# Optimization experiments

Hardware: AMD Instinct MI355X
Metric: run time of the kernel (lower is better)

## Reference

```python
import jax, jax.numpy as jnp
import numpy as np

NHID = 128; NUM_CLASSES = 128; NUM_CONVS = 3; EDGE_RATIO = 0.8
B_GRAPHS = 256; N_PER_G = 256; E_PER_G = 512
N_TOTAL = B_GRAPHS * N_PER_G; E_TOTAL = B_GRAPHS * E_PER_G
ATOM_DIMS = [119, 4, 12, 12, 10, 6, 6, 2, 2]
BOND_DIMS = [5, 6, 2]


def setup_inputs():
    key = jax.random.key(0)
    ks = jax.random.split(key, 32)
    a_off = np.concatenate([[0], np.cumsum(ATOM_DIMS)[:-1]])
    x_idx = jnp.stack([jax.random.randint(ks[i], (N_TOTAL,), 0, dm) + int(o)
                       for i, (dm, o) in enumerate(zip(ATOM_DIMS, a_off))], axis=1)
    b_off = np.concatenate([[0], np.cumsum(BOND_DIMS)[:-1]])
    edge_attr_idx = jnp.stack([jax.random.randint(ks[9 + i], (E_TOTAL,), 0, dm) + int(o)
                               for i, (dm, o) in enumerate(zip(BOND_DIMS, b_off))], axis=1)
    # block-structured edges: each graph's edges are contiguous, endpoints local
    src = jax.random.randint(ks[12], (B_GRAPHS, E_PER_G), 0, N_PER_G)
    dst = jax.random.randint(ks[13], (B_GRAPHS, E_PER_G), 0, N_PER_G)
    off = jnp.arange(B_GRAPHS)[:, None] * N_PER_G
    edge_index = jnp.stack([(src + off).reshape(-1), (dst + off).reshape(-1)])
    batch = jnp.repeat(jnp.arange(B_GRAPHS), N_PER_G)
    s = 0.05
    d = NHID
    def rn(k, shape):
        return jax.random.normal(k, shape, dtype=jnp.float32) * s
    return {
        "x_idx": x_idx, "edge_attr_idx": edge_attr_idx,
        "edge_index": edge_index, "batch": batch,
        "atom_table": rn(ks[14], (sum(ATOM_DIMS), d)),
        "bond_table": rn(ks[15], (sum(BOND_DIMS), d)),
        "W_gcn": rn(ks[16], (NUM_CONVS, d, d)), "b_gcn": rn(ks[17], (NUM_CONVS, d)),
        "root_emb": rn(ks[18], (NUM_CONVS, d)),
        "W_hyp": rn(ks[19], (NUM_CONVS - 1, d, d)), "b_hyp": rn(ks[20], (NUM_CONVS - 1, d)),
        "W_sc": rn(ks[21], (NUM_CONVS - 1, d, 1)), "b_sc": rn(ks[22], (NUM_CONVS - 1, 1)),
        "Wc1": rn(ks[23], (3 * d, d)), "bc1": rn(ks[24], (d,)),
        "Wc2": rn(ks[25], (d, d // 2)), "bc2": rn(ks[26], (d // 2,)),
        "Wc3": rn(ks[27], (d // 2, NUM_CLASSES)), "bc3": rn(ks[28], (NUM_CLASSES,)),
    }


def reference(x_idx, edge_attr_idx, edge_index, batch, atom_table, bond_table,
              W_gcn, b_gcn, root_emb, W_hyp, b_hyp, W_sc, b_sc,
              Wc1, bc1, Wc2, bc2, Wc3, bc3):
    seg = jax.ops.segment_sum
    x = atom_table[x_idx].sum(axis=1)          # [N, d] AtomEncoder: sum of per-feature embeddings
    e = bond_table[edge_attr_idx].sum(axis=1)  # [E, d] BondEncoder
    edge_weight = None
    xs = 0.0
    for l in range(NUM_CONVS):
        E = edge_index.shape[1]
        # ---- DHT: dual hypergraph (edges -> nodes, nodes -> hyperedges), with loops & degree-1 mask
        flat = edge_index.T.reshape(-1)  # [2E] node ids in (src,dst,src,dst,...) order
        node_idx = jnp.concatenate([jnp.repeat(jnp.arange(E), 2), jnp.arange(E)])       # [3E]
        hyper_idx = jnp.concatenate([flat, N_TOTAL + jnp.arange(E)])                    # [3E]
        bc = seg(jnp.ones(2 * E, jnp.float32), flat, num_segments=N_TOTAL)
        mask = jnp.concatenate([bc[flat] != 1.0, jnp.ones((E,), dtype=bool)])
        w = mask.astype(x.dtype)
        NH = N_TOTAL + E
        # ---- GCNConv_OGB
        row, col = edge_index[0], edge_index[1]
        h = x @ W_gcn[l] + b_gcn[l]
        deg = seg(jnp.ones(E, x.dtype), row, num_segments=N_TOTAL) + 1.0
        dis = deg ** -0.5
        msg = (dis[row] * dis[col])[:, None] * jax.nn.relu(h[row] + e)
        if edge_weight is not None:
            msg = msg * edge_weight[:, None]
        x = jax.nn.relu(seg(msg, col, num_segments=N_TOTAL)
                        + jax.nn.relu(h + root_emb[l]) / deg[:, None])
        if l < NUM_CONVS - 1:
            # ---- HypergraphConv on edge features (nodes of dual = original edges)
            Dn = seg(w, node_idx, num_segments=E)
            Bh = seg(w, hyper_idx, num_segments=NH)
            Dinv = jnp.where(Dn > 0, 1.0 / Dn, 0.0)
            Binv = jnp.where(Bh > 0, 1.0 / Bh, 0.0)
            def hconv(feat, W, b):
                z = feat @ W
                m = seg(z[node_idx] * w[:, None], hyper_idx, num_segments=NH) * Binv[:, None]
                return seg(m[hyper_idx] * w[:, None], node_idx, num_segments=E) * Dinv[:, None] + b
            e = jax.nn.relu(hconv(e, W_hyp[l], b_hyp[l]))
            score = jnp.tanh(hconv(e, W_sc[l], b_sc[l]).squeeze(-1))  # [E]
            # ---- topk edge pooling (uniform per-graph blocks -> static k)
            Eg = E // B_GRAPHS
            k = int(np.ceil(EDGE_RATIO * Eg))
            _, loc = jax.lax.top_k(score.reshape(B_GRAPHS, Eg), k)
            perm = (loc + jnp.arange(B_GRAPHS)[:, None] * Eg).reshape(-1)
            edge_index = edge_index[:, perm]
            e = e[perm]
            edge_weight = jnp.clip(score[perm], 0.0, 1.0)
        # ---- readout: gmp | gap | gsp  (uniform graphs -> reshape)
        xr = x.reshape(B_GRAPHS, N_PER_G, NHID)
        xs = xs + jnp.concatenate([xr.max(axis=1), xr.mean(axis=1), xr.sum(axis=1)], axis=1)
    # ---- classifier (eval mode: dropout is identity)
    h1 = jax.nn.relu(xs @ Wc1 + bc1)
    h2 = jax.nn.relu(h1 @ Wc2 + bc2)
    return h2 @ Wc3 + bc3
```

## Files before the change

kernel.cpp:

```cpp
#include <hip/hip_runtime.h>
#include <hip/hip_bf16.h>
#include <math.h>

constexpr int NTOT = 65536;
constexpr int D    = 128;
constexpr int BG   = 256;
constexpr int E0 = 131072, E1 = 104960, E2 = 83968;
constexpr int EG0 = 512;
constexpr int KP0 = 410, KP1 = 328;

typedef __bf16 bf16x8 __attribute__((ext_vector_type(8)));
typedef __bf16 bf16x4 __attribute__((ext_vector_type(4)));
typedef __bf16 bf16x2 __attribute__((ext_vector_type(2)));
typedef float  f32x4  __attribute__((ext_vector_type(4)));

__device__ __forceinline__ float2 tof2(bf16x2 v) {
  return make_float2((float)v[0], (float)v[1]);
}
__device__ __forceinline__ bf16x2 tob2(float ax, float ay) {
  bf16x2 r; r[0] = (__bf16)ax; r[1] = (__bf16)ay; return r;
}

__global__ __launch_bounds__(256) void k_embed_x(const int* __restrict__ xi,
                                                 const float* __restrict__ tab,
                                                 __bf16* __restrict__ x) {
  int t = blockIdx.x * 256 + threadIdx.x;
  int v = t >> 5, q = (t & 31) << 2;
  float4 s = {0.f, 0.f, 0.f, 0.f};
#pragma unroll
  for (int j = 0; j < 9; ++j) {
    int r = xi[v * 9 + j];
    float4 a = *(const float4*)&tab[r * D + q];
    s.x += a.x; s.y += a.y; s.z += a.z; s.w += a.w;
  }
  bf16x4 o; o[0] = (__bf16)s.x; o[1] = (__bf16)s.y; o[2] = (__bf16)s.z; o[3] = (__bf16)s.w;
  *(bf16x4*)&x[(size_t)v * D + q] = o;
}

__global__ __launch_bounds__(256) void k_embed_e(const int* __restrict__ bi,
                                                 const float* __restrict__ tab,
                                                 __bf16* __restrict__ e) {
  int t = blockIdx.x * 256 + threadIdx.x;
  int i = t >> 5, q = (t & 31) << 2;
  float4 s = {0.f, 0.f, 0.f, 0.f};
#pragma unroll
  for (int j = 0; j < 3; ++j) {
    int r = bi[i * 3 + j];
    float4 a = *(const float4*)&tab[r * D + q];
    s.x += a.x; s.y += a.y; s.z += a.z; s.w += a.w;
  }
  bf16x4 o; o[0] = (__bf16)s.x; o[1] = (__bf16)s.y; o[2] = (__bf16)s.z; o[3] = (__bf16)s.w;
  *(bf16x4*)&e[(size_t)i * D + q] = o;
}

__global__ __launch_bounds__(256) void k_gemm_bf16(const __bf16* __restrict__ A,
                                                   const float* __restrict__ W,
                                                   const float* __restrict__ bias,
                                                   __bf16* __restrict__ C) {
  __shared__ bf16x8 Wl[4][8][64];
  const int t = threadIdx.x, w = t >> 6, lane = t & 63;
  const int m0 = blockIdx.x * 128;

  bf16x8* Wf = (bf16x8*)Wl;
  for (int q = t; q < 2048; q += 256) {
    int ks = q >> 9, nt = (q >> 6) & 7, l = q & 63;
    int kk = ks * 32 + ((l >> 4) << 3);
    int nn = nt * 16 + (l & 15);
    const float* wp = W + (size_t)kk * 128 + nn;
    bf16x8 v;
#pragma unroll
    for (int b = 0; b < 8; ++b) v[b] = (__bf16)wp[(size_t)b * 128];
    Wf[q] = v;
  }

  const int r0 = m0 + w * 32 + (lane & 15);
  const __bf16* Ap0 = A + (size_t)r0 * 128 + ((lane >> 4) << 3);
  const __bf16* Ap1 = Ap0 + 16 * 128;
  bf16x8 a0[4], a1[4];
#pragma unroll
  for (int ks = 0; ks < 4; ++ks) {
    a0[ks] = *(const bf16x8*)(Ap0 + ks * 32);
    a1[ks] = *(const bf16x8*)(Ap1 + ks * 32);
  }
  __syncthreads();

  f32x4 acc0[8] = {}; f32x4 acc1[8] = {};
#pragma unroll
  for (int ks = 0; ks < 4; ++ks) {
#pragma unroll
    for (int nt = 0; nt < 8; ++nt) {
      bf16x8 b = Wl[ks][nt][lane];
      acc0[nt] = __builtin_amdgcn_mfma_f32_16x16x32_bf16(a0[ks], b, acc0[nt], 0, 0, 0);
      acc1[nt] = __builtin_amdgcn_mfma_f32_16x16x32_bf16(a1[ks], b, acc1[nt], 0, 0, 0);
    }
  }

  const int orow = m0 + w * 32 + ((lane >> 4) << 2);
  const int ocol = lane & 15;
#pragma unroll
  for (int nt = 0; nt < 8; ++nt) {
    float bb = bias ? bias[nt * 16 + ocol] : 0.f;
    __bf16* cp = C + (size_t)orow * 128 + nt * 16 + ocol;
#pragma unroll
    for (int r = 0; r < 4; ++r) {
      cp[(size_t)r * 128]        = (__bf16)(acc0[nt][r] + bb);
      cp[(size_t)(16 + r) * 128] = (__bf16)(acc1[nt][r] + bb);
    }
  }
}

template <int EG, bool HAS_EW>
__global__ __launch_bounds__(1024, 4) void k_gcn_fused(const int* __restrict__ ei, int E,
                                                       const __bf16* __restrict__ e,
                                                       const float* __restrict__ Wg,
                                                       const float* __restrict__ bg,
                                                       const float* __restrict__ ew,
                                                       const float* __restrict__ root,
                                                       __bf16* __restrict__ x,
                                                       float* __restrict__ xs) {
  constexpr int NW = 16;
  __shared__ bf16x8 Wl[4][8][64];
  __shared__ __bf16 hl[256 * 128];
  __shared__ int   pke[EG];
  __shared__ float coef[EG];
  __shared__ int   cnts[256];
  __shared__ int   cntd[256];
  __shared__ int   off[257];
  __shared__ int   cur[256];
  __shared__ int   wsum[4];
  __shared__ short adj[EG];
  __shared__ float redm[16 * 128], reds[16 * 128];
  const int g = blockIdx.x;
  const int t = threadIdx.x, w = t >> 6, lane = t & 63;
  const bf16x2* eg2 = (const bf16x2*)e + (size_t)g * EG * 64 + lane;
  bf16x2* xg2 = (bf16x2*)x + (size_t)g * 256 * 64 + lane;

  if (t < 256) { cnts[t] = 0; cntd[t] = 0; }
  __syncthreads();

  for (int j = t; j < EG; j += 1024) {
    int s = ei[g * EG + j] & 255, d = ei[E + g * EG + j] & 255;
    pke[j] = s | (d << 8);
    atomicAdd(&cnts[s], 1);
    atomicAdd(&cntd[d], 1);
  }
  {
    bf16x8* Wf = (bf16x8*)Wl;
    for (int q = t; q < 2048; q += 1024) {
      int ks = q >> 9, nt = (q >> 6) & 7, l = q & 63;
      int kk = ks * 32 + ((l >> 4) << 3);
      int nn = nt * 16 + (l & 15);
      const float* wp = Wg + (size_t)kk * 128 + nn;
      bf16x8 v;
#pragma unroll
      for (int b = 0; b < 8; ++b) v[b] = (__bf16)wp[(size_t)b * 128];
      Wf[q] = v;
    }
  }
  __syncthreads();

  {
    const int r0 = w * 16 + (lane & 15);
    const __bf16* Ap = x + ((size_t)(g * 256 + r0)) * 128 + ((lane >> 4) << 3);
    bf16x8 af[4];
#pragma unroll
    for (int ks = 0; ks < 4; ++ks) af[ks] = *(const bf16x8*)(Ap + ks * 32);
    f32x4 acc[8] = {};
#pragma unroll
    for (int ks = 0; ks < 4; ++ks) {
#pragma unroll
      for (int nt = 0; nt < 8; ++nt) {
        acc[nt] = __builtin_amdgcn_mfma_f32_16x16x32_bf16(af[ks], Wl[ks][nt][lane], acc[nt], 0, 0, 0);
      }
    }
    const int lrow = w * 16 + ((lane >> 4) << 2);
    const int ocol = lane & 15;
#pragma unroll
    for (int nt = 0; nt < 8; ++nt) {
      float bb = bg[nt * 16 + ocol];
#pragma unroll
      for (int r = 0; r < 4; ++r)
        hl[(lrow + r) * 128 + nt * 16 + ocol] = (__bf16)(acc[nt][r] + bb);
    }
  }

  for (int j = t; j < EG; j += 1024) {
    int p = pke[j];
    int s = p & 255, d = (p >> 8) & 255;
    float c = rsqrtf(((float)cnts[s] + 1.f) * ((float)cnts[d] + 1.f));
    if (HAS_EW) c *= ew[g * EG + j];
    coef[j] = c;
  }

  {
    int v = 0;
    if (t < 256) {
      v = cntd[t];
#pragma unroll
      for (int d2 = 1; d2 < 64; d2 <<= 1) {
        int u = __shfl_up(v, d2);
        if (lane >= d2) v += u;
      }
      if (lane == 63) wsum[w] = v;
    }
    __syncthreads();
    if (t < 256) {
      int add = 0;
      if (w > 0) add += wsum[0];
      if (w > 1) add += wsum[1];
      if (w > 2) add += wsum[2];
      off[t + 1] = v + add;
      if (t == 0) off[0] = 0;
      cur[t] = v + add - cntd[t];
    }
    __syncthreads();
  }

  for (int j = t; j < EG; j += 1024) {
    int d = (pke[j] >> 8) & 255;
    int pos = atomicAdd(&cur[d], 1);
    adj[pos] = (short)j;
  }
  __syncthreads();

  const float rvx = root[2 * lane], rvy = root[2 * lane + 1];
  float2 mx = {-1e30f, -1e30f}, sm = {0.f, 0.f};
  for (int n = w; n < 256; n += NW) {
    float2 val = {0.f, 0.f};
    int b0 = off[n], b1 = off[n + 1];
    int k = b0;
    for (; k + 1 < b1; k += 2) {
      int j0 = adj[k], j1 = adj[k + 1];
      int s0 = pke[j0] & 255, s1 = pke[j1] & 255;
      float2 e0 = tof2(eg2[(size_t)j0 * 64]), e1 = tof2(eg2[(size_t)j1 * 64]);
      float2 h0 = tof2(*(const bf16x2*)&hl[s0 * 128 + 2 * lane]);
      float2 h1 = tof2(*(const bf16x2*)&hl[s1 * 128 + 2 * lane]);
      float c0 = coef[j0], c1 = coef[j1];
      val.x += c0 * fmaxf(h0.x + e0.x, 0.f) + c1 * fmaxf(h1.x + e1.x, 0.f);
      val.y += c0 * fmaxf(h0.y + e0.y, 0.f) + c1 * fmaxf(h1.y + e1.y, 0.f);
    }
    if (k < b1) {
      int j0 = adj[k];
      int s0 = pke[j0] & 255;
      float2 e0 = tof2(eg2[(size_t)j0 * 64]);
      float2 h0 = tof2(*(const bf16x2*)&hl[s0 * 128 + 2 * lane]);
      float c0 = coef[j0];
      val.x += c0 * fmaxf(h0.x + e0.x, 0.f);
      val.y += c0 * fmaxf(h0.y + e0.y, 0.f);
    }
    float inv = 1.f / ((float)cnts[n] + 1.f);
    float2 hv = tof2(*(const bf16x2*)&hl[n * 128 + 2 * lane]);
    float xvx = fmaxf(val.x + fmaxf(hv.x + rvx, 0.f) * inv, 0.f);
    float xvy = fmaxf(val.y + fmaxf(hv.y + rvy, 0.f) * inv, 0.f);
    xg2[(size_t)n * 64] = tob2(xvx, xvy);
    mx.x = fmaxf(mx.x, xvx); mx.y = fmaxf(mx.y, xvy);
    sm.x += xvx;             sm.y += xvy;
  }
  redm[w * 128 + 2 * lane]     = mx.x;
  redm[w * 128 + 2 * lane + 1] = mx.y;
  reds[w * 128 + 2 * lane]     = sm.x;
  reds[w * 128 + 2 * lane + 1] = sm.y;
  __syncthreads();

  if (t < 128) {
    float M = redm[t], S2 = reds[t];
#pragma unroll
    for (int k = 1; k < 16; ++k) {
      M = fmaxf(M, redm[k * 128 + t]);
      S2 += reds[k * 128 + t];
    }
    xs[g * 384 + t]       += M;
    xs[g * 384 + 128 + t] += S2 * (1.f / 256.f);
    xs[g * 384 + 256 + t] += S2;
  }
}

template <int EG, int KEEP, int ENEW>
__global__ __launch_bounds__(1024, 4) void k_hyper_sort(const int* __restrict__ ei, int E,
                                                        const __bf16* __restrict__ z,
                                                        const float* __restrict__ bias,
                                                        const float* __restrict__ wsc,
                                                        const float* __restrict__ bsc,
                                                        __bf16* __restrict__ eout,
                                                        int* __restrict__ ei_new,
                                                        __bf16* __restrict__ e_new,
                                                        float* __restrict__ ew) {
  constexpr int NW = 16;
  __shared__ __bf16 S[256 * 128];
  __shared__ int   pke[EG];
  __shared__ float as_[EG], ad_[EG], az_[EG];
  __shared__ float zsh[EG];
  __shared__ float Ssh[256];
  __shared__ int   cnt[256];
  __shared__ int   off[257];
  __shared__ int   cur[256];
  __shared__ int   wsum[4];
  __shared__ short adj[2 * EG];
  __shared__ float ls[512];
  __shared__ int   li[512];
  __shared__ int   sidx[512];
  const int g = blockIdx.x;
  const int t = threadIdx.x, w = t >> 6, lane = t & 63;
  const bf16x2* zg2 = (const bf16x2*)z + (size_t)g * EG * 64 + lane;
  bf16x2* eo2 = (bf16x2*)eout + (size_t)g * EG * 64 + lane;
  bf16x2* S2 = (bf16x2*)S;

  if (t < 256) { cnt[t] = 0; Ssh[t] = 0.f; }
  __syncthreads();

  for (int j = t; j < EG; j += 1024) {
    int s = ei[g * EG + j] & 255, d = ei[E + g * EG + j] & 255;
    pke[j] = s | (d << 8);
    atomicAdd(&cnt[s], 1);
    atomicAdd(&cnt[d], 1);
  }
  __syncthreads();

  for (int j = t; j < EG; j += 1024) {
    int p = pke[j];
    int s = p & 255, d = (p >> 8) & 255;
    int cs = cnt[s], cd = cnt[d];
    float bis  = (cs != 1) ? 1.f / (float)cs : 0.f;
    float bid_ = (cd != 1) ? 1.f / (float)cd : 0.f;
    float dinv = 1.f / (1.f + (cs != 1 ? 1.f : 0.f) + (cd != 1 ? 1.f : 0.f));
    as_[j] = dinv * bis;
    ad_[j] = dinv * bid_;
    az_[j] = dinv;
  }

  {
    int v = 0;
    if (t < 256) {
      v = cnt[t];
#pragma unroll
      for (int d2 = 1; d2 < 64; d2 <<= 1) {
        int u = __shfl_up(v, d2);
        if (lane >= d2) v += u;
      }
      if (lane == 63) wsum[w] = v;
    }
    __syncthreads();
    if (t < 256) {
      int add = 0;
      if (w > 0) add += wsum[0];
      if (w > 1) add += wsum[1];
      if (w > 2) add += wsum[2];
      off[t + 1] = v + add;
      if (t == 0) off[0] = 0;
      cur[t] = v + add - cnt[t];
    }
    __syncthreads();
  }

  for (int j = t; j < EG; j += 1024) {
    int p = pke[j];
    int pos0 = atomicAdd(&cur[p & 255], 1);
    adj[pos0] = (short)j;
    int pos1 = atomicAdd(&cur[(p >> 8) & 255], 1);
    adj[pos1] = (short)j;
  }
  __syncthreads();

  for (int n = w; n < 256; n += NW) {
    float2 val = {0.f, 0.f};
    int b0 = off[n], b1 = off[n + 1];
    int k = b0;
    for (; k + 1 < b1; k += 2) {
      float2 a = tof2(zg2[(size_t)adj[k] * 64]);
      float2 b = tof2(zg2[(size_t)adj[k + 1] * 64]);
      val.x += a.x + b.x;
      val.y += a.y + b.y;
    }
    if (k < b1) {
      float2 a = tof2(zg2[(size_t)adj[k] * 64]);
      val.x += a.x; val.y += a.y;
    }
    S2[n * 64 + lane] = tob2(val.x, val.y);
  }
  __syncthreads();

  const float bbx = bias[2 * lane], bby = bias[2 * lane + 1];
  const float wvx = wsc[2 * lane],  wvy = wsc[2 * lane + 1];
  for (int j = w; j < EG; j += NW) {
    int p = pke[j];
    int s = p & 255, d = (p >> 8) & 255;
    float a_s = as_[j], a_d = ad_[j], a_z = az_[j];
    float2 Sv = tof2(S2[s * 64 + lane]);
    float2 Dv = tof2(S2[d * 64 + lane]);
    float2 zv = tof2(zg2[(size_t)j * 64]);
    float ox = fmaxf(a_s * Sv.x + a_d * Dv.x + a_z * zv.x + bbx, 0.f);
    float oy = fmaxf(a_s * Sv.y + a_d * Dv.y + a_z * zv.y + bby, 0.f);
    eo2[(size_t)j * 64] = tob2(ox, oy);
    float part = ox * wvx + oy * wvy;
#pragma unroll
    for (int offs = 32; offs > 0; offs >>= 1) part += __shfl_xor(part, offs);
    if (lane == 0) zsh[j] = part;
  }
  __syncthreads();

  if (t < EG) {
    float v = zsh[t];
    atomicAdd(&Ssh[pke[t] & 255], v);
    atomicAdd(&Ssh[(pke[t] >> 8) & 255], v);
  }
  __syncthreads();

  float sc = -INFINITY; int idx = 0x7FFFFFFF;
  if (t < EG) {
    int p = pke[t];
    int sn = p & 255, dn = (p >> 8) & 255;
    sc = tanhf(as_[t] * Ssh[sn] + ad_[t] * Ssh[dn] + az_[t] * zsh[t] + bsc[0]);
    idx = t;
  }
#pragma unroll
  for (int k = 2; k <= 512; k <<= 1) {
#pragma unroll
    for (int j = k >> 1; j > 0; j >>= 1) {
      if (j < 64) {
        if (t < 512) {
          float ps = __shfl_xor(sc, j);
          int   pi = __shfl_xor(idx, j);
          bool ownBetter = (sc > ps) || (sc == ps && idx < pi);
          bool lower = ((t & j) == 0);
          bool desc = ((t & k) == 0);
          bool keep = desc ? (lower ? ownBetter : !ownBetter)
                           : (lower ? !ownBetter : ownBetter);
          if (!keep) { sc = ps; idx = pi; }
        }
      } else {
        if (t < 512) { ls[t] = sc; li[t] = idx; }
        __syncthreads();
        if (t < 512) {
          float ps = ls[t ^ j];
          int   pi = li[t ^ j];
          bool ownBetter = (sc > ps) || (sc == ps && idx < pi);
          bool lower = ((t & j) == 0);
          bool desc = ((t & k) == 0);
          bool keep = desc ? (lower ? ownBetter : !ownBetter)
                           : (lower ? !ownBetter : ownBetter);
          if (!keep) { sc = ps; idx = pi; }
        }
        __syncthreads();
      }
    }
  }

  if (t < 512) sidx[t] = idx;
  if (t < KEEP) {
    int oldp = g * EG + idx;
    int newp = g * KEEP + t;
    ei_new[newp]        = ei[oldp];
    ei_new[ENEW + newp] = ei[E + oldp];
    ew[newp] = fminf(fmaxf(sc, 0.f), 1.f);
  }
  __syncthreads();

  const float4* src = (const float4*)eout;
  float4* dst = (float4*)e_new;
  for (int q = t; q < KEEP * 16; q += 1024) {
    int j2 = q >> 4, c = q & 15;
    dst[((size_t)g * KEEP + j2) * 16 + c] = src[((size_t)g * EG + sidx[j2]) * 16 + c];
  }
}

__global__ __launch_bounds__(128) void k_mlp(const float* __restrict__ xs,
                                             const float* __restrict__ Wc1, const float* __restrict__ bc1,
                                             const float* __restrict__ Wc2, const float* __restrict__ bc2,
                                             const float* __restrict__ Wc3, const float* __restrict__ bc3,
                                             float* __restrict__ out) {
  __shared__ float row[384];
  __shared__ float h1[128];
  __shared__ float h2[64];
  int g = blockIdx.x, t = threadIdx.x;
  for (int i = t; i < 384; i += 128) row[i] = xs[g * 384 + i];
  __syncthreads();
  float a = bc1[t];
  for (int k = 0; k < 384; ++k) a += row[k] * Wc1[k * 128 + t];
  h1[t] = fmaxf(a, 0.f);
  __syncthreads();
  if (t < 64) {
    float b = bc2[t];
    for (int k = 0; k < 128; ++k) b += h1[k] * Wc2[k * 64 + t];
    h2[t] = fmaxf(b, 0.f);
  }
  __syncthreads();
  float o = bc3[t];
  for (int k = 0; k < 64; ++k) o += h2[k] * Wc3[k * 128 + t];
  out[g * 128 + t] = o;
}

extern "C" void kernel_launch(void* const* d_in, const int* in_sizes, int n_in,
                              void* d_out, int out_size, void* d_ws, size_t ws_size,
                              hipStream_t stream) {
  (void)in_sizes; (void)n_in; (void)out_size; (void)ws_size;
  const int*   x_idx  = (const int*)d_in[0];
  const int*   b_idx  = (const int*)d_in[1];
  const int*   ei0    = (const int*)d_in[2];
  const float* atom_t = (const float*)d_in[4];
  const float* bond_t = (const float*)d_in[5];
  const float* W_gcn  = (const float*)d_in[6];
  const float* b_gcn  = (const float*)d_in[7];
  const float* root   = (const float*)d_in[8];
  const float* W_hyp  = (const float*)d_in[9];
  const float* b_hyp  = (const float*)d_in[10];
  const float* W_sc   = (const float*)d_in[11];
  const float* b_sc   = (const float*)d_in[12];
  const float* Wc1    = (const float*)d_in[13];
  const float* bc1_   = (const float*)d_in[14];
  const float* Wc2    = (const float*)d_in[15];
  const float* bc2_   = (const float*)d_in[16];
  const float* Wc3    = (const float*)d_in[17];
  const float* bc3_   = (const float*)d_in[18];
  float* out = (float*)d_out;

  __bf16* x  = (__bf16*)d_ws;
  __bf16* eA = x  + (size_t)NTOT * D;
  __bf16* eB = eA + (size_t)E0 * D;
  float* ew  = (float*)(eB + (size_t)E0 * D);
  float* xs  = ew + E0;
  int*   eiB  = (int*)(xs + BG * 384);
  int*   eiA2 = eiB + 2 * E0;

  hipMemsetAsync(xs, 0, BG * 384 * 4, stream);
  k_embed_x<<<NTOT * 32 / 256, 256, 0, stream>>>(x_idx, atom_t, x);
  k_embed_e<<<E0 * 32 / 256, 256, 0, stream>>>(b_idx, bond_t, eA);

  k_gcn_fused<EG0, false><<<BG, 1024, 0, stream>>>(ei0, E0, eA, W_gcn, b_gcn, nullptr, root, x, xs);
  k_gemm_bf16<<<E0 / 128, 256, 0, stream>>>(eA, W_hyp, nullptr, eB);
  k_hyper_sort<EG0, KP0, E1><<<BG, 1024, 0, stream>>>(ei0, E0, eB, b_hyp, W_sc, b_sc, eA, eiB, eB, ew);

  k_gcn_fused<KP0, true><<<BG, 1024, 0, stream>>>(eiB, E1, eB, W_gcn + D * D, b_gcn + D, ew, root + D, x, xs);
  k_gemm_bf16<<<E1 / 128, 256, 0, stream>>>(eB, W_hyp + D * D, nullptr, eA);
  k_hyper_sort<KP0, KP1, E2><<<BG, 1024, 0, stream>>>(eiB, E1, eA, b_hyp + D, W_sc + D, b_sc + 1, eB, eiA2, eA, ew);

  k_gcn_fused<KP1, true><<<BG, 1024, 0, stream>>>(eiA2, E2, eA, W_gcn + 2 * D * D, b_gcn + 2 * D, ew, root + 2 * D, x, xs);

  k_mlp<<<BG, 128, 0, stream>>>(xs, Wc1, bc1_, Wc2, bc2_, Wc3, bc3_, out);
}
```

Measured before the change: 251.9 us.

## Fuse hypergraph linear GEMM into per-graph hyper_sort kernel

After: 225.1 us. -10.6%, faster.

```diff
diff --git a/kernel.cpp b/kernel.cpp
--- a/kernel.cpp
+++ b/kernel.cpp
@@ -51,62 +51,6 @@
   }
   bf16x4 o; o[0] = (__bf16)s.x; o[1] = (__bf16)s.y; o[2] = (__bf16)s.z; o[3] = (__bf16)s.w;
   *(bf16x4*)&e[(size_t)i * D + q] = o;
-}
-
-__global__ __launch_bounds__(256) void k_gemm_bf16(const __bf16* __restrict__ A,
-                                                   const float* __restrict__ W,
-                                                   const float* __restrict__ bias,
-                                                   __bf16* __restrict__ C) {
-  __shared__ bf16x8 Wl[4][8][64];
-  const int t = threadIdx.x, w = t >> 6, lane = t & 63;
-  const int m0 = blockIdx.x * 128;
-
-  bf16x8* Wf = (bf16x8*)Wl;
-  for (int q = t; q < 2048; q += 256) {
-    int ks = q >> 9, nt = (q >> 6) & 7, l = q & 63;
-    int kk = ks * 32 + ((l >> 4) << 3);
-    int nn = nt * 16 + (l & 15);
-    const float* wp = W + (size_t)kk * 128 + nn;
-    bf16x8 v;
-#pragma unroll
-    for (int b = 0; b < 8; ++b) v[b] = (__bf16)wp[(size_t)b * 128];
-    Wf[q] = v;
-  }
-
-  const int r0 = m0 + w * 32 + (lane & 15);
-  const __bf16* Ap0 = A + (size_t)r0 * 128 + ((lane >> 4) << 3);
-  const __bf16* Ap1 = Ap0 + 16 * 128;
-  bf16x8 a0[4], a1[4];
-#pragma unroll
-  for (int ks = 0; ks < 4; ++ks) {
-    a0[ks] = *(const bf16x8*)(Ap0 + ks * 32);
-    a1[ks] = *(const bf16x8*)(Ap1 + ks * 32);
-  }
-  __syncthreads();
-
-  f32x4 acc0[8] = {}; f32x4 acc1[8] = {};
-#pragma unroll
-  for (int ks = 0; ks < 4; ++ks) {
-#pragma unroll
-    for (int nt = 0; nt < 8; ++nt) {
-      bf16x8 b = Wl[ks][nt][lane];
-      acc0[nt] = __builtin_amdgcn_mfma_f32_16x16x32_bf16(a0[ks], b, acc0[nt], 0, 0, 0);
-      acc1[nt] = __builtin_amdgcn_mfma_f32_16x16x32_bf16(a1[ks], b, acc1[nt], 0, 0, 0);
-    }
-  }
-
-  const int orow = m0 + w * 32 + ((lane >> 4) << 2);
-  const int ocol = lane & 15;
-#pragma unroll
-  for (int nt = 0; nt < 8; ++nt) {
-    float bb = bias ? bias[nt * 16 + ocol] : 0.f;
-    __bf16* cp = C + (size_t)orow * 128 + nt * 16 + ocol;
-#pragma unroll
-    for (int r = 0; r < 4; ++r) {
-      cp[(size_t)r * 128]        = (__bf16)(acc0[nt][r] + bb);
-      cp[(size_t)(16 + r) * 128] = (__bf16)(acc1[nt][r] + bb);
-    }
-  }
 }
 
 template <int EG, bool HAS_EW>
@@ -277,15 +221,17 @@
 
 template <int EG, int KEEP, int ENEW>
 __global__ __launch_bounds__(1024, 4) void k_hyper_sort(const int* __restrict__ ei, int E,
-                                                        const __bf16* __restrict__ z,
+                                                        __bf16* __restrict__ e,
+                                                        const float* __restrict__ Wh,
                                                         const float* __restrict__ bias,
                                                         const float* __restrict__ wsc,
                                                         const float* __restrict__ bsc,
-                                                        __bf16* __restrict__ eout,
+                                                        __bf16* __restrict__ zbuf,
                                                         int* __restrict__ ei_new,
                                                         __bf16* __restrict__ e_new,
                                                         float* __restrict__ ew) {
   constexpr int NW = 16;
+  __shared__ bf16x8 Wl[4][8][64];
   __shared__ __bf16 S[256 * 128];
   __shared__ int   pke[EG];
   __shared__ float as_[EG], ad_[EG], az_[EG];
@@ -301,8 +247,8 @@
   __shared__ int   sidx[512];
   const int g = blockIdx.x;
   const int t = threadIdx.x, w = t >> 6, lane = t & 63;
-  const bf16x2* zg2 = (const bf16x2*)z + (size_t)g * EG * 64 + lane;
-  bf16x2* eo2 = (bf16x2*)eout + (size_t)g * EG * 64 + lane;
+  const bf16x2* zg2 = (const bf16x2*)zbuf + (size_t)g * EG * 64 + lane;
+  bf16x2* eo2 = (bf16x2*)e + (size_t)g * EG * 64 + lane;
   bf16x2* S2 = (bf16x2*)S;
 
   if (t < 256) { cnt[t] = 0; Ssh[t] = 0.f; }
@@ -314,7 +260,57 @@
     atomicAdd(&cnt[s], 1);
     atomicAdd(&cnt[d], 1);
   }
-  __syncthreads();
+  {
+    bf16x8* Wf = (bf16x8*)Wl;
+    for (int q = t; q < 2048; q += 1024) {
+      int ks = q >> 9, nt = (q >> 6) & 7, l = q & 63;
+      int kk = ks * 32 + ((l >> 4) << 3);
+      int nn = nt * 16 + (l & 15);
+      const float* wp = Wh + (size_t)kk * 128 + nn;
+      bf16x8 v;
+#pragma unroll
+      for (int b = 0; b < 8; ++b) v[b] = (__bf16)wp[(size_t)b * 128];
+      Wf[q] = v;
+    }
+  }
+  const int r0 = w * 32 + (lane & 15);
+  const int r1 = r0 + 16;
+  bf16x8 a0[4], a1[4];
+  {
+    bf16x8 zz = {};
+    const __bf16* Ap0 = e + ((size_t)g * EG + r0) * 128 + ((lane >> 4) << 3);
+    const __bf16* Ap1 = Ap0 + (size_t)16 * 128;
+#pragma unroll
+    for (int ks = 0; ks < 4; ++ks) {
+      a0[ks] = (r0 < EG) ? *(const bf16x8*)(Ap0 + ks * 32) : zz;
+      a1[ks] = (r1 < EG) ? *(const bf16x8*)(Ap1 + ks * 32) : zz;
+    }
+  }
+  __syncthreads();
+
+  {
+    f32x4 acc0[8] = {}; f32x4 acc1[8] = {};
+#pragma unroll
+    for (int ks = 0; ks < 4; ++ks) {
+#pragma unroll
+      for (int nt = 0; nt < 8; ++nt) {
+        bf16x8 b = Wl[ks][nt][lane];
+        acc0[nt] = __builtin_amdgcn_mfma_f32_16x16x32_bf16(a0[ks], b, acc0[nt], 0, 0, 0);
+        acc1[nt] = __builtin_amdgcn_mfma_f32_16x16x32_bf16(a1[ks], b, acc1[nt], 0, 0, 0);
+      }
+    }
+    const int orow = w * 32 + ((lane >> 4) << 2);
+    const int ocol = lane & 15;
+#pragma unroll
+    for (int nt = 0; nt < 8; ++nt) {
+      __bf16* zp = zbuf + ((size_t)g * EG + orow) * 128 + nt * 16 + ocol;
+#pragma unroll
+      for (int r = 0; r < 4; ++r) {
+        if (orow + r < EG)      zp[(size_t)r * 128]        = (__bf16)acc0[nt][r];
+        if (orow + 16 + r < EG) zp[(size_t)(16 + r) * 128] = (__bf16)acc1[nt][r];
+      }
+    }
+  }
 
   for (int j = t; j < EG; j += 1024) {
     int p = pke[j];
@@ -455,7 +451,7 @@
   }
   __syncthreads();
 
-  const float4* src = (const float4*)eout;
+  const float4* src = (const float4*)e;
   float4* dst = (float4*)e_new;
   for (int q = t; q < KEEP * 16; q += 1024) {
     int j2 = q >> 4, c = q & 15;
@@ -513,10 +509,11 @@
   const float* bc3_   = (const float*)d_in[18];
   float* out = (float*)d_out;
 
-  __bf16* x  = (__bf16*)d_ws;
-  __bf16* eA = x  + (size_t)NTOT * D;
-  __bf16* eB = eA + (size_t)E0 * D;
-  float* ew  = (float*)(eB + (size_t)E0 * D);
+  __bf16* x    = (__bf16*)d_ws;
+  __bf16* eA   = x    + (size_t)NTOT * D;
+  __bf16* eB   = eA   + (size_t)E0 * D;
+  __bf16* zbuf = eB   + (size_t)E0 * D;
+  float* ew  = (float*)(zbuf + (size_t)E0 * D);
   float* xs  = ew + E0;
   int*   eiB  = (int*)(xs + BG * 384);
   int*   eiA2 = eiB + 2 * E0;
@@ -526,12 +523,10 @@
   k_embed_e<<<E0 * 32 / 256, 256, 0, stream>>>(b_idx, bond_t, eA);
 
   k_gcn_fused<EG0, false><<<BG, 1024, 0, stream>>>(ei0, E0, eA, W_gcn, b_gcn, nullptr, root, x, xs);
-  k_gemm_bf16<<<E0 / 128, 256, 0, stream>>>(eA, W_hyp, nullptr, eB);
-  k_hyper_sort<EG0, KP0, E1><<<BG, 1024, 0, stream>>>(ei0, E0, eB, b_hyp, W_sc, b_sc, eA, eiB, eB, ew);
+  k_hyper_sort<EG0, KP0, E1><<<BG, 1024, 0, stream>>>(ei0, E0, eA, W_hyp, b_hyp, W_sc, b_sc, zbuf, eiB, eB, ew);
 
   k_gcn_fused<KP0, true><<<BG, 1024, 0, stream>>>(eiB, E1, eB, W_gcn + D * D, b_gcn + D, ew, root + D, x, xs);
-  k_gemm_bf16<<<E1 / 128, 256, 0, stream>>>(eB, W_hyp + D * D, nullptr, eA);
-  k_hyper_sort<KP0, KP1, E2><<<BG, 1024, 0, stream>>>(eiB, E1, eA, b_hyp + D, W_sc + D, b_sc + 1, eB, eiA2, eA, ew);
+  k_hyper_sort<KP0, KP1, E2><<<BG, 1024, 0, stream>>>(eiB, E1, eB, W_hyp + D * D, b_hyp + D, W_sc + D, b_sc + 1, zbuf, eiA2, eA, ew);
 
   k_gcn_fused<KP1, true><<<BG, 1024, 0, stream>>>(eiA2, E2, eA, W_gcn + 2 * D * D, b_gcn + 2 * D, ew, root + 2 * D, x, xs);
 
```
